# Performance work log

Measured on AMD Instinct MI355X. Metric: run time of the kernel, lower is better.

Reference implementation:

```python
import jax, jax.numpy as jnp
import numpy as np

N_NODES, N_EDGES, BATCH_SIZE = 8192, 65536, 64
N_S, NG, MAX_R = 16, 32, 10.0
SQRT3 = float(np.sqrt(3.0))


def _mlp2(h, w1, b1, w2, b2):
    return jax.nn.relu(h @ w1 + b1) @ w2 + b2


def _mlp3(h, w1, b1, w2, b2, w3, b3):
    h = jax.nn.relu(h @ w1 + b1)
    h = jax.nn.relu(h @ w2 + b2)
    return h @ w3 + b3


def _scatter_mean(vals, idx, n):
    s = jax.ops.segment_sum(vals, idx, num_segments=n)
    c = jax.ops.segment_sum(jnp.ones(vals.shape[:1], vals.dtype), idx, num_segments=n)
    return s / jnp.maximum(c, 1.0)[:, None]


def _forward_molecule(x, pos, src, dst, batch, params):
    (ne_w1, ne_b1, ne_w2, ne_b2, ee_w1, ee_b1, ee_w2, ee_b2,
     c0_w1, c0_b1, c0_w2, c0_b2, c1_w1, c1_b1, c1_w2, c1_b2,
     sn_w1, sn_b1, sn_w2, sn_b2, sn_w3, sn_b3,
     se_w1, se_b1, se_w2, se_b2, se_w3, se_b3) = params
    n = x.shape[0]
    evec = pos[dst] - pos[src]                       # [E,3]
    dist = jnp.sqrt(jnp.sum(evec * evec, -1) + 1e-12)
    mu = jnp.linspace(0.0, MAX_R, NG)
    coeff = -0.5 / (MAX_R / (NG - 1)) ** 2           # GaussianSmearing
    edge_attr = jnp.exp(coeff * (dist[:, None] - mu) ** 2)     # [E,NG]
    sh1 = SQRT3 * evec / dist[:, None]               # l=1 SH, component norm; l=0 part == 1

    h = _mlp2(x, ne_w1, ne_b1, ne_w2, ne_b2)         # node embedding [N,16]
    eemb = _mlp2(edge_attr, ee_w1, ee_b1, ee_w2, ee_b2)        # edge embedding [E,16]

    # ---- conv 0: 16x0e (x) 0e+1o -> 16x0e+16x1o, per-edge TP weights ----
    ea = jnp.concatenate([eemb, h[dst, :N_S], h[src, :N_S]], -1)   # [E,48]
    w = _mlp2(ea, c0_w1, c0_b1, c0_w2, c0_b2)                      # [E,512]
    E = w.shape[0]
    w00 = w[:, :256].reshape(E, 16, 16)    # 0e x 0e -> 0e
    w01 = w[:, 256:].reshape(E, 16, 16)    # 0e x 1o -> 1o
    xs = h[src]
    o0 = 0.25 * jnp.einsum('eu,euw->ew', xs, w00)        # path weight 1/sqrt(16)
    o1 = 0.25 * jnp.einsum('eu,em,euw->ewm', xs, sh1, w01)
    tp = jnp.concatenate([o0, o1.reshape(E, 48)], -1)
    up = _scatter_mean(tp, dst, n)                       # [N,64]
    h = jnp.pad(h, ((0, 0), (0, up.shape[1] - h.shape[1]))) + up

    # ---- conv 1: 16x0e+16x1o (x) 0e+1o -> 16x0e+16x1o+16x1e ----
    ea = jnp.concatenate([eemb, h[dst, :N_S], h[src, :N_S]], -1)
    w = _mlp2(ea, c1_w1, c1_b1, c1_w2, c1_b2)                      # [E,1280]
    wA, wB, wC, wD, wE = (w[:, i * 256:(i + 1) * 256].reshape(E, 16, 16) for i in range(5))
    x0s = h[src, :16]
    x1s = h[src, 16:64].reshape(E, 16, 3)
    pw = 1.0 / float(np.sqrt(32.0))        # two fan-16 paths into 0e and into 1o
    o0 = pw * (jnp.einsum('eu,euw->ew', x0s, wA)
               + jnp.einsum('eui,ei,euw->ew', x1s, sh1, wD) / SQRT3)  # CG(1,1,0)=delta/sqrt3
    o1o = pw * (jnp.einsum('eu,em,euw->ewm', x0s, sh1, wB)
                + jnp.einsum('eum,euw->ewm', x1s, wC))
    cr = jnp.cross(x1s, sh1[:, None, :])                              # CG(1,1,1)=eps/sqrt2
    o1e = (0.25 / float(np.sqrt(2.0))) * jnp.einsum('euk,euw->ewk', cr, wE)
    tp = jnp.concatenate([o0, o1o.reshape(E, 48), o1e.reshape(E, 48)], -1)
    up = _scatter_mean(tp, dst, n)                       # [N,112]
    h = jnp.pad(h, ((0, 0), (0, up.shape[1] - h.shape[1]))) + up

    xf = h[:, :N_S]                                      # n_conv_layers < 3 branch
    s_nodes = _mlp3(xf, sn_w1, sn_b1, sn_w2, sn_b2, sn_w3, sn_b3)   # [N,1]
    s_edges = _mlp3(jnp.concatenate([edge_attr, xf[src], xf[dst]], -1),
                    se_w1, se_b1, se_w2, se_b2, se_w3, se_b3)       # [E,1]
    # edge_in_score=True -> edge and node scatter_add into per-molecule score
    return (jax.ops.segment_sum(s_edges, batch[src], num_segments=BATCH_SIZE)
            + jax.ops.segment_sum(s_nodes, batch, num_segments=BATCH_SIZE))


def setup_inputs() -> dict:
    ks = iter(jax.random.split(jax.random.key(0), 64))

    def nrm(shape, scale=1.0):
        return scale * jax.random.normal(next(ks), shape, jnp.float32)

    def lin(fi, fo):
        return nrm((fi, fo), 1.0 / float(np.sqrt(fi)))

    def z(n):
        return jnp.zeros((n,), jnp.float32)

    inp = {}
    for tag in ('r', 'p'):
        inp[f'x_{tag}'] = nrm((N_NODES, 32))
        inp[f'pos_{tag}'] = 2.0 * jax.random.normal(next(ks), (N_NODES, 3), jnp.float32)
        s = jax.random.randint(next(ks), (N_EDGES,), 0, N_NODES)
        o = jax.random.randint(next(ks), (N_EDGES,), 1, N_NODES)   # no self loops
        inp[f'edge_index_{tag}'] = jnp.stack([s, (s + o) % N_NODES]).astype(jnp.int32)
        inp[f'batch_{tag}'] = jnp.sort(jax.random.randint(next(ks), (N_NODES,), 0, BATCH_SIZE)).astype(jnp.int32)
    inp['ne_w1'] = lin(32, 16); inp['ne_b1'] = z(16); inp['ne_w2'] = lin(16, 16); inp['ne_b2'] = z(16)
    inp['ee_w1'] = lin(32, 16); inp['ee_b1'] = z(16); inp['ee_w2'] = lin(16, 16); inp['ee_b2'] = z(16)
    inp['c0_w1'] = lin(48, 48); inp['c0_b1'] = z(48); inp['c0_w2'] = lin(48, 512); inp['c0_b2'] = z(512)
    inp['c1_w1'] = lin(48, 48); inp['c1_b1'] = z(48); inp['c1_w2'] = lin(48, 1280); inp['c1_b2'] = z(1280)
    inp['sn_w1'] = lin(16, 32); inp['sn_b1'] = z(32); inp['sn_w2'] = lin(32, 16); inp['sn_b2'] = z(16)
    inp['sn_w3'] = lin(16, 1); inp['sn_b3'] = z(1)
    inp['se_w1'] = lin(64, 16); inp['se_b1'] = z(16); inp['se_w2'] = lin(16, 16); inp['se_b2'] = z(16)
    inp['se_w3'] = lin(16, 1); inp['se_b3'] = z(1)
    return inp


def reference(x_r, pos_r, edge_index_r, batch_r, x_p, pos_p, edge_index_p, batch_p,
              ne_w1, ne_b1, ne_w2, ne_b2, ee_w1, ee_b1, ee_w2, ee_b2,
              c0_w1, c0_b1, c0_w2, c0_b2, c1_w1, c1_b1, c1_w2, c1_b2,
              sn_w1, sn_b1, sn_w2, sn_b2, sn_w3, sn_b3,
              se_w1, se_b1, se_w2, se_b2, se_w3, se_b3):
    params = (ne_w1, ne_b1, ne_w2, ne_b2, ee_w1, ee_b1, ee_w2, ee_b2,
              c0_w1, c0_b1, c0_w2, c0_b2, c1_w1, c1_b1, c1_w2, c1_b2,
              sn_w1, sn_b1, sn_w2, sn_b2, sn_w3, sn_b3,
              se_w1, se_b1, se_w2, se_b2, se_w3, se_b3)
    e_r = _forward_molecule(x_r, pos_r, edge_index_r[0], edge_index_r[1], batch_r, params)
    e_p = _forward_molecule(x_p, pos_p, edge_index_p[0], edge_index_p[1], batch_p, params)
    return e_p - e_r   # reaction energy [BATCH_SIZE, 1]
```

## Files before the change

### kernel.cpp

```cpp
#include <hip/hip_runtime.h>
#include <math.h>

#define NN 8192
#define NE 65536
#define SQRT3F 1.7320508075688772f
#define INV_SQRT3F 0.5773502691896258f
#define PW 0.17677669529663687f
#define GSTEP (10.0f/31.0f)
#define GCOEFF (-0.5f/(GSTEP*GSTEP))

typedef _Float16 f16;
typedef f16 f16x2 __attribute__((ext_vector_type(2)));
typedef f16 f16x4 __attribute__((ext_vector_type(4)));
typedef f16 f16x8 __attribute__((ext_vector_type(8)));
typedef float f32x4 __attribute__((ext_vector_type(4)));

#define MFMA(acc, a, b) acc = __builtin_amdgcn_mfma_f32_16x16x32_f16(a, b, acc, 0, 0, 0)

__global__ __launch_bounds__(256) void k_pre(const float* __restrict__ c0w1, const float* __restrict__ c0b1,
                                             const float* __restrict__ c1w1, const float* __restrict__ c1b1,
                                             const float* __restrict__ c0w2, const float* __restrict__ c0b2,
                                             const float* __restrict__ c1w2, const float* __restrict__ c1b2,
                                             f16* __restrict__ w1c0, f16* __restrict__ w1c1,
                                             f16* __restrict__ w2t0, f16* __restrict__ w2t1,
                                             const float* __restrict__ xr, const float* __restrict__ xp,
                                             float* __restrict__ h16f, f16* __restrict__ h16_16,
                                             const float* __restrict__ nw1, const float* __restrict__ nb1,
                                             const float* __restrict__ nw2, const float* __restrict__ nb2,
                                             const int* __restrict__ eir, const int* __restrict__ eip,
                                             const float* __restrict__ posr, const float* __restrict__ posp,
                                             float* __restrict__ sh1d, f16* __restrict__ eemb16,
                                             int* __restrict__ cnt,
                                             const float* __restrict__ ew1, const float* __restrict__ eb1,
                                             const float* __restrict__ ew2, const float* __restrict__ eb2) {
    int b = blockIdx.x;
    int tid = threadIdx.x;
    if (b < 320) {
        int idx = b * 256 + tid;
        if (idx >= 1280 * 64) return;
        int n = idx >> 6, h = idx & 63;
        w2t1[idx] = (f16)((h < 48) ? c1w2[h * 1280 + n] : (h == 48 ? c1b2[n] : 0.f));
        if (n < 512) w2t0[idx] = (f16)((h < 48) ? c0w2[h * 512 + n] : (h == 48 ? c0b2[n] : 0.f));
        if (n < 48) {
            w1c0[idx] = (f16)((h < 48) ? c0w1[h * 48 + n] : (h == 48 ? c0b1[n] : 0.f));
            w1c1[idx] = (f16)((h < 48) ? c1w1[h * 48 + n] : (h == 48 ? c1b1[n] : 0.f));
        }
    } else if (b < 384) {
        int bb = b - 320;
        int mol = bb >> 5;
        const float* x = mol ? xp : xr;
        float* hf = h16f + (size_t)mol * NN * 16;
        f16* h16o = h16_16 + (size_t)mol * NN * 16;
        int v = (bb & 31) * 256 + tid;
        float xi[32];
#pragma unroll
        for (int i = 0; i < 32; i++) xi[i] = x[v * 32 + i];
        float a[16];
#pragma unroll
        for (int j = 0; j < 16; j++) a[j] = nb1[j];
#pragma unroll
        for (int i = 0; i < 32; i++)
#pragma unroll
            for (int j = 0; j < 16; j++) a[j] = fmaf(xi[i], nw1[i * 16 + j], a[j]);
#pragma unroll
        for (int j = 0; j < 16; j++) a[j] = fmaxf(a[j], 0.f);
        float o[16];
#pragma unroll
        for (int j = 0; j < 16; j++) o[j] = nb2[j];
#pragma unroll
        for (int i = 0; i < 16; i++)
#pragma unroll
            for (int j = 0; j < 16; j++) o[j] = fmaf(a[i], nw2[i * 16 + j], o[j]);
#pragma unroll
        for (int j = 0; j < 16; j++) { hf[v * 16 + j] = o[j]; h16o[v * 16 + j] = (f16)o[j]; }
    } else {
        int bb = b - 384;
        int mol = bb >> 8;
        const int* ei = mol ? eip : eir;
        const float* pos = mol ? posp : posr;
        float* sh_ = sh1d + (size_t)mol * NE * 4;
        f16* em_ = eemb16 + (size_t)mol * NE * 16;
        int* cn_ = cnt + mol * NN;
        int e = (bb & 255) * 256 + tid;
        int s = ei[e], d = ei[NE + e];
        float ex = pos[d * 3 + 0] - pos[s * 3 + 0];
        float ey = pos[d * 3 + 1] - pos[s * 3 + 1];
        float ez = pos[d * 3 + 2] - pos[s * 3 + 2];
        float dist = sqrtf(ex * ex + ey * ey + ez * ez + 1e-12f);
        float inv = SQRT3F / dist;
        sh_[e * 4 + 0] = ex * inv;
        sh_[e * 4 + 1] = ey * inv;
        sh_[e * 4 + 2] = ez * inv;
        sh_[e * 4 + 3] = dist;
        float g[32];
#pragma unroll
        for (int i = 0; i < 32; i++) {
            float t = dist - (float)i * GSTEP;
            g[i] = __expf(GCOEFF * t * t);
        }
        float a[16];
#pragma unroll
        for (int j = 0; j < 16; j++) a[j] = eb1[j];
#pragma unroll
        for (int i = 0; i < 32; i++)
#pragma unroll
            for (int j = 0; j < 16; j++) a[j] = fmaf(g[i], ew1[i * 16 + j], a[j]);
#pragma unroll
        for (int j = 0; j < 16; j++) a[j] = fmaxf(a[j], 0.f);
        float o[16];
#pragma unroll
        for (int j = 0; j < 16; j++) o[j] = eb2[j];
#pragma unroll
        for (int i = 0; i < 16; i++)
#pragma unroll
            for (int j = 0; j < 16; j++) o[j] = fmaf(a[i], ew2[i * 16 + j], o[j]);
#pragma unroll
        for (int j = 0; j < 16; j++) em_[e * 16 + j] = (f16)o[j];
        atomicAdd(&cn_[d], 1);
    }
}

__global__ __launch_bounds__(256) void k_scan(int* __restrict__ cnt, int* __restrict__ rowptr,
                                              float* __restrict__ out) {
    __shared__ int part[256];
    int mol = blockIdx.x;
    int* c = cnt + mol * NN;
    int* rp = rowptr + mol * (NN + 1);
    int t = threadIdx.x;
    int base = t * (NN / 256);
    int s = 0;
#pragma unroll
    for (int i = 0; i < NN / 256; i++) s += c[base + i];
    part[t] = s;
    __syncthreads();
    if (t == 0) {
        int run = 0;
        for (int i = 0; i < 256; i++) { int v = part[i]; part[i] = run; run += v; }
    }
    __syncthreads();
    int run = part[t];
    for (int i = 0; i < NN / 256; i++) {
        int cv = c[base + i];
        rp[base + i] = run;
        run += cv;
        c[base + i] = 0;
    }
    if (t == 255) rp[NN] = run;
    if (mol == 0 && t < 64) out[t] = 0.f;
}

__global__ __launch_bounds__(256) void k_fill(const int* __restrict__ eir, const int* __restrict__ eip,
                                              const int* __restrict__ rowptr, int* __restrict__ cnt,
                                              int* __restrict__ eord) {
    int mol = blockIdx.y;
    const int* ei = mol ? eip : eir;
    int e = blockIdx.x * 256 + threadIdx.x;
    int d = ei[NE + e];
    int pos = atomicAdd(&cnt[mol * NN + d], 1);
    eord[mol * NE + rowptr[mol * (NN + 1) + d] + pos] = e;
}

__global__ __launch_bounds__(128) void k_conv0(const int* __restrict__ eir, const int* __restrict__ eip,
                                               const int* __restrict__ eord,
                                               const f16* __restrict__ eemb16, const f16* __restrict__ h16_16,
                                               const float* __restrict__ sh1d,
                                               const f16* __restrict__ w1h, const f16* __restrict__ w2h,
                                               f16* __restrict__ tp0) {
    __shared__ __align__(16) f16 ea[256 * 72];
    __shared__ __align__(16) f16 sc0[256 * 24];
    __shared__ __align__(16) float4 shs[256];
    int mol = blockIdx.y;
    const int* ei = mol ? eip : eir;
    const int* eo = eord + mol * NE;
    const f16* em_ = eemb16 + (size_t)mol * NE * 16;
    const f16* h16_ = h16_16 + (size_t)mol * NN * 16;
    const float* sh_ = sh1d + (size_t)mol * NE * 4;
    f16* tp_ = tp0 + (size_t)mol * NE * 64;
    int tid = threadIdx.x;
    int e0 = blockIdx.x * 256;
#pragma unroll
    for (int ii = 0; ii < 2; ii++) {
        int er = tid * 2 + ii;
        int le = eo[e0 + er];
        int s = ei[le], d = ei[NE + le];
        char* row = (char*)ea + er * 144;
        const f16x8* pe = (const f16x8*)(em_ + (size_t)le * 16);
        ((f16x8*)row)[0] = pe[0]; ((f16x8*)row)[1] = pe[1];
        const f16x8* pd = (const f16x8*)(h16_ + (size_t)d * 16);
        ((f16x8*)row)[2] = pd[0]; ((f16x8*)row)[3] = pd[1];
        const f16x8* ps = (const f16x8*)(h16_ + (size_t)s * 16);
        f16x8 sv0 = ps[0], sv1 = ps[1];
        ((f16x8*)row)[4] = sv0; ((f16x8*)row)[5] = sv1;
        f16x8 z = {}; f16x8 o = {}; o[0] = (f16)1.0f;
        ((f16x8*)row)[6] = o; ((f16x8*)row)[7] = z; ((f16x8*)row)[8] = z;
        char* srow = (char*)sc0 + er * 48;
        *(f16x8*)srow = sv0;
        *(f16x8*)(srow + 16) = sv1;
        shs[er] = *(const float4*)(sh_ + (size_t)le * 4);
    }
    int wv = tid >> 6, l = tid & 63;
    int koff = (l >> 4) * 16;
    int voffB = (l & 15) * 128 + koff;
    int rbase = wv * 128;
#pragma unroll
    for (int t = 0; t < 8; t++) {
        int arow = rbase + t * 16 + (l & 15);
        f16x8 a0 = *(const f16x8*)((const char*)ea + arow * 144 + koff);
        f16x8 a1 = *(const f16x8*)((const char*)ea + arow * 144 + koff + 64);
#pragma unroll
        for (int nt = 0; nt < 3; nt++) {
            f32x4 hacc = {0.f, 0.f, 0.f, 0.f};
            const char* hb = (const char*)w1h + nt * 2048 + voffB;
            MFMA(hacc, a0, *(const f16x8*)(hb));
            MFMA(hacc, a1, *(const f16x8*)(hb + 64));
#pragma unroll
            for (int r = 0; r < 4; r++) {
                int rr = rbase + t * 16 + (l >> 4) * 4 + r;
                ea[rr * 72 + nt * 16 + (l & 15)] = (f16)fmaxf(hacc[r], 0.f);
            }
        }
    }
    f16x8 ha0[8], ha1[8];
#pragma unroll
    for (int t = 0; t < 8; t++) {
        int arow = rbase + t * 16 + (l & 15);
        ha0[t] = *(const f16x8*)((const char*)ea + arow * 144 + koff);
        ha1[t] = *(const f16x8*)((const char*)ea + arow * 144 + koff + 64);
    }
    f32x4 accA[8] = {}, accB[8] = {};
    const char* wB = (const char*)w2h + voffB;
    f16x8 cA0 = *(const f16x8*)(wB), cA1 = *(const f16x8*)(wB + 64);
    f16x8 cB0 = *(const f16x8*)(wB + 32768), cB1 = *(const f16x8*)(wB + 32768 + 64);
#pragma unroll 4
    for (int u = 0; u < 16; ++u) {
        int un = (u < 15) ? u + 1 : 15;
        const char* Hb = wB + un * 2048;
        f16x8 nA0 = *(const f16x8*)(Hb), nA1 = *(const f16x8*)(Hb + 64);
        f16x8 nB0 = *(const f16x8*)(Hb + 32768), nB1 = *(const f16x8*)(Hb + 32768 + 64);
#pragma unroll
        for (int t = 0; t < 8; t++) {
            f16 s = *(const f16*)((const char*)sc0 + (rbase + t * 16 + (l & 15)) * 48 + u * 2);
            f16x8 x0 = ha0[t] * s, x1 = ha1[t] * s;
            MFMA(accA[t], x0, cA0); MFMA(accA[t], x1, cA1);
            MFMA(accB[t], x0, cB0); MFMA(accB[t], x1, cB1);
        }
        cA0 = nA0; cA1 = nA1; cB0 = nB0; cB1 = nB1;
    }
    int w = l & 15;
#pragma unroll
    for (int t = 0; t < 8; t++)
#pragma unroll
        for (int r = 0; r < 4; r++) {
            int ro = rbase + t * 16 + (l >> 4) * 4 + r;
            int i = e0 + ro;
            float4 shv = shs[ro];
            f16* tpp = tp_ + (size_t)i * 64;
            float tb = 0.25f * accB[t][r];
            tpp[w] = (f16)(0.25f * accA[t][r]);
            tpp[16 + w] = (f16)(tb * shv.x);
            tpp[32 + w] = (f16)(tb * shv.y);
            tpp[48 + w] = (f16)(tb * shv.z);
        }
}

__global__ __launch_bounds__(256) void k_up0g(const float* __restrict__ h16f, const f16* __restrict__ tp0,
                                              const int* __restrict__ rowptr,
                                              float* __restrict__ h64f, f16* __restrict__ h64_16) {
    int mol = blockIdx.y;
    const float* h_ = h16f + (size_t)mol * NN * 16;
    const f16* tp = tp0 + (size_t)mol * NE * 64;
    const int* rp = rowptr + mol * (NN + 1);
    float* o_ = h64f + (size_t)mol * NN * 64;
    f16* o16_ = h64_16 + (size_t)mol * NN * 16;
    int tid = threadIdx.x;
    int v = blockIdx.x * 64 + (tid >> 2), q = tid & 3;
    int r0 = rp[v], r1 = rp[v + 1];
    float acc[16];
#pragma unroll
    for (int j = 0; j < 16; j++) acc[j] = 0.f;
    for (int i = r0; i < r1; i++) {
        const f16* src = tp + (size_t)i * 64 + q * 16;
        f16x8 v0 = *(const f16x8*)src;
        f16x8 v1 = *(const f16x8*)(src + 8);
#pragma unroll
        for (int j = 0; j < 8; j++) { acc[j] += (float)v0[j]; acc[8 + j] += (float)v1[j]; }
    }
    float rc = 1.0f / fmaxf((float)(r1 - r0), 1.0f);
    if (q == 0) {
#pragma unroll
        for (int w = 0; w < 16; w++) {
            float val = fmaf(acc[w], rc, h_[(size_t)v * 16 + w]);
            o_[(size_t)v * 64 + w] = val;
            o16_[(size_t)v * 16 + w] = (f16)val;
        }
    } else {
#pragma unroll
        for (int w = 0; w < 16; w++) o_[(size_t)v * 64 + 16 + 3 * w + (q - 1)] = acc[w] * rc;
    }
}

__global__ __launch_bounds__(128) void k_conv1(const int* __restrict__ eir, const int* __restrict__ eip,
                                               const int* __restrict__ eord,
                                               const f16* __restrict__ eemb16, const f16* __restrict__ h64_16,
                                               const float* __restrict__ h64f, const float* __restrict__ sh1d,
                                               const f16* __restrict__ w1h, const f16* __restrict__ w2h,
                                               f16* __restrict__ tp1) {
    __shared__ __align__(16) f16 ea[256 * 72];
    __shared__ __align__(16) f16 sc1[256 * 36];
    int mol = blockIdx.y;
    const int* ei = mol ? eip : eir;
    const int* eo = eord + mol * NE;
    const f16* em_ = eemb16 + (size_t)mol * NE * 16;
    const f16* h16_ = h64_16 + (size_t)mol * NN * 16;
    const float* hf_ = h64f + (size_t)mol * NN * 64;
    const float* sh_ = sh1d + (size_t)mol * NE * 4;
    f16* tp_ = tp1 + (size_t)mol * NE * 16;
    int tid = threadIdx.x;
    int e0 = blockIdx.x * 256;
#pragma unroll
    for (int ii = 0; ii < 2; ii++) {
        int er = tid * 2 + ii;
        int le = eo[e0 + er];
        int s = ei[le], d = ei[NE + le];
        char* row = (char*)ea + er * 144;
        const f16x8* pe = (const f16x8*)(em_ + (size_t)le * 16);
        ((f16x8*)row)[0] = pe[0]; ((f16x8*)row)[1] = pe[1];
        const f16x8* pd = (const f16x8*)(h16_ + (size_t)d * 16);
        ((f16x8*)row)[2] = pd[0]; ((f16x8*)row)[3] = pd[1];
        const f16x8* ps = (const f16x8*)(h16_ + (size_t)s * 16);
        ((f16x8*)row)[4] = ps[0]; ((f16x8*)row)[5] = ps[1];
        f16x8 z = {}; f16x8 o = {}; o[0] = (f16)1.0f;
        ((f16x8*)row)[6] = o; ((f16x8*)row)[7] = z; ((f16x8*)row)[8] = z;
        float4 shv = *(const float4*)(sh_ + (size_t)le * 4);
        const float* hfs = hf_ + (size_t)s * 64;
        float xu[16];
#pragma unroll
        for (int g = 0; g < 4; g++) {
            float4 v4 = *(const float4*)(hfs + g * 4);
            xu[g * 4 + 0] = v4.x; xu[g * 4 + 1] = v4.y; xu[g * 4 + 2] = v4.z; xu[g * 4 + 3] = v4.w;
        }
        float x1v[48];
#pragma unroll
        for (int g = 0; g < 12; g++) {
            float4 v4 = *(const float4*)(hfs + 16 + g * 4);
            x1v[g * 4 + 0] = v4.x; x1v[g * 4 + 1] = v4.y; x1v[g * 4 + 2] = v4.z; x1v[g * 4 + 3] = v4.w;
        }
        char* srow = (char*)sc1 + er * 72;
#pragma unroll
        for (int g = 0; g < 4; g++) {
            f16x8 pk;
#pragma unroll
            for (int k2 = 0; k2 < 4; k2++) {
                int k = g * 4 + k2;
                float du = (x1v[k * 3] * shv.x + x1v[k * 3 + 1] * shv.y + x1v[k * 3 + 2] * shv.z) * INV_SQRT3F;
                pk[k2 * 2 + 0] = (f16)xu[k];
                pk[k2 * 2 + 1] = (f16)du;
            }
            *(f16x8*)(srow + g * 16) = pk;
        }
    }
    int wv = tid >> 6, l = tid & 63;
    int koff = (l >> 4) * 16;
    int voffB = (l & 15) * 128 + koff;
    int rbase = wv * 128;
#pragma unroll
    for (int t = 0; t < 8; t++) {
        int arow = rbase + t * 16 + (l & 15);
        f16x8 a0 = *(const f16x8*)((const char*)ea + arow * 144 + koff);
        f16x8 a1 = *(const f16x8*)((const char*)ea + arow * 144 + koff + 64);
#pragma unroll
        for (int nt = 0; nt < 3; nt++) {
            f32x4 hacc = {0.f, 0.f, 0.f, 0.f};
            const char* hb = (const char*)w1h + nt * 2048 + voffB;
            MFMA(hacc, a0, *(const f16x8*)(hb));
            MFMA(hacc, a1, *(const f16x8*)(hb + 64));
#pragma unroll
            for (int r = 0; r < 4; r++) {
                int rr = rbase + t * 16 + (l >> 4) * 4 + r;
                ea[rr * 72 + nt * 16 + (l & 15)] = (f16)fmaxf(hacc[r], 0.f);
            }
        }
    }
    f16x8 ha0[8], ha1[8];
#pragma unroll
    for (int t = 0; t < 8; t++) {
        int arow = rbase + t * 16 + (l & 15);
        ha0[t] = *(const f16x8*)((const char*)ea + arow * 144 + koff);
        ha1[t] = *(const f16x8*)((const char*)ea + arow * 144 + koff + 64);
    }
    f32x4 accA[8] = {};
    const char* wB = (const char*)w2h + voffB;
    f16x8 cA0 = *(const f16x8*)(wB), cA1 = *(const f16x8*)(wB + 64);
    f16x8 cD0 = *(const f16x8*)(wB + 98304), cD1 = *(const f16x8*)(wB + 98304 + 64);
#pragma unroll 4
    for (int u = 0; u < 16; ++u) {
        int un = (u < 15) ? u + 1 : 15;
        const char* Hb = wB + un * 2048;
        f16x8 nA0 = *(const f16x8*)(Hb), nA1 = *(const f16x8*)(Hb + 64);
        f16x8 nD0 = *(const f16x8*)(Hb + 98304), nD1 = *(const f16x8*)(Hb + 98304 + 64);
#pragma unroll
        for (int t = 0; t < 8; t++) {
            f16x2 sp = *(const f16x2*)((const char*)sc1 + (rbase + t * 16 + (l & 15)) * 72 + u * 4);
            f16x8 x0 = ha0[t] * sp[0], x1 = ha1[t] * sp[0];
            MFMA(accA[t], x0, cA0); MFMA(accA[t], x1, cA1);
            x0 = ha0[t] * sp[1]; x1 = ha1[t] * sp[1];
            MFMA(accA[t], x0, cD0); MFMA(accA[t], x1, cD1);
        }
        cA0 = nA0; cA1 = nA1; cD0 = nD0; cD1 = nD1;
    }
    int w = l & 15;
#pragma unroll
    for (int t = 0; t < 8; t++)
#pragma unroll
        for (int r = 0; r < 4; r++) {
            int i = e0 + rbase + t * 16 + (l >> 4) * 4 + r;
            tp_[(size_t)i * 16 + w] = (f16)(PW * accA[t][r]);
        }
}

__global__ __launch_bounds__(256) void k_xfg(const float* __restrict__ h64f, const f16* __restrict__ tp1,
                                             const int* __restrict__ rowptr,
                                             float* __restrict__ xf,
                                             const int* __restrict__ batchr, const int* __restrict__ batchp,
                                             const float* __restrict__ w1, const float* __restrict__ b1,
                                             const float* __restrict__ w2, const float* __restrict__ b2,
                                             const float* __restrict__ w3, const float* __restrict__ b3,
                                             float* __restrict__ out) {
    __shared__ float xfs[64][17];
    __shared__ float buck[64];
    int tid = threadIdx.x;
    if (tid < 64) buck[tid] = 0.f;
    int mol = blockIdx.y;
    float sign = mol ? 1.f : -1.f;
    const int* batch = mol ? batchp : batchr;
    const float* h_ = h64f + (size_t)mol * NN * 64;
    const f16* tp = tp1 + (size_t)mol * NE * 16;
    const int* rp = rowptr + mol * (NN + 1);
    float* xf_ = xf + (size_t)mol * NN * 16;
    int v = blockIdx.x * 64 + (tid >> 2), q = tid & 3;
    int r0 = rp[v], r1 = rp[v + 1];
    float a0 = 0.f, a1 = 0.f, a2 = 0.f, a3 = 0.f;
    for (int i = r0; i < r1; i++) {
        f16x4 t4 = *(const f16x4*)(tp + (size_t)i * 16 + q * 4);
        a0 += (float)t4[0]; a1 += (float)t4[1]; a2 += (float)t4[2]; a3 += (float)t4[3];
    }
    float rc = 1.0f / fmaxf((float)(r1 - r0), 1.0f);
    float4 hv = *(const float4*)(h_ + (size_t)v * 64 + q * 4);
    float4 xv4;
    xv4.x = fmaf(a0, rc, hv.x); xv4.y = fmaf(a1, rc, hv.y);
    xv4.z = fmaf(a2, rc, hv.z); xv4.w = fmaf(a3, rc, hv.w);
    xfs[tid >> 2][q * 4 + 0] = xv4.x; xfs[tid >> 2][q * 4 + 1] = xv4.y;
    xfs[tid >> 2][q * 4 + 2] = xv4.z; xfs[tid >> 2][q * 4 + 3] = xv4.w;
    *(float4*)(xf_ + (size_t)v * 16 + q * 4) = xv4;
    __syncthreads();
    if (tid < 64) {
        int v2 = blockIdx.x * 64 + tid;
        float xv[16];
#pragma unroll
        for (int c = 0; c < 16; c++) xv[c] = xfs[tid][c];
        float aa[32];
#pragma unroll
        for (int j = 0; j < 32; j++) aa[j] = b1[j];
#pragma unroll
        for (int i = 0; i < 16; i++)
#pragma unroll
            for (int j = 0; j < 32; j++) aa[j] = fmaf(xv[i], w1[i * 32 + j], aa[j]);
#pragma unroll
        for (int j = 0; j < 32; j++) aa[j] = fmaxf(aa[j], 0.f);
        float bb[16];
#pragma unroll
        for (int j = 0; j < 16; j++) bb[j] = b2[j];
#pragma unroll
        for (int i = 0; i < 32; i++)
#pragma unroll
            for (int j = 0; j < 16; j++) bb[j] = fmaf(aa[i], w2[i * 16 + j], bb[j]);
#pragma unroll
        for (int j = 0; j < 16; j++) bb[j] = fmaxf(bb[j], 0.f);
        float val = b3[0];
#pragma unroll
        for (int i = 0; i < 16; i++) val = fmaf(bb[i], w3[i], val);
        atomicAdd(&buck[batch[v2]], val);
    }
    __syncthreads();
    if (tid < 64) atomicAdd(&out[tid], sign * buck[tid]);
}

__global__ __launch_bounds__(256) void k_sedge(const int* __restrict__ eir, const int* __restrict__ eip,
                                               const int* __restrict__ batchr, const int* __restrict__ batchp,
                                               const float* __restrict__ sh1d, const float* __restrict__ xf,
                                               const float* __restrict__ w1, const float* __restrict__ b1,
                                               const float* __restrict__ w2, const float* __restrict__ b2,
                                               const float* __restrict__ w3, const float* __restrict__ b3,
                                               float* __restrict__ out) {
    __shared__ float buck[64];
    int tid = threadIdx.x;
    if (tid < 64) buck[tid] = 0.f;
    __syncthreads();
    int mol = blockIdx.y;
    float sign = mol ? 1.f : -1.f;
    const int* ei = mol ? eip : eir;
    const int* batch = mol ? batchp : batchr;
    const float* sh_ = sh1d + (size_t)mol * NE * 4;
    const float* xf_ = xf + (size_t)mol * NN * 16;
    int e = blockIdx.x * 256 + tid;
    int s = ei[e], d = ei[NE + e];
    float dist = sh_[e * 4 + 3];
    float in[64];
#pragma unroll
    for (int i = 0; i < 32; i++) {
        float t = dist - (float)i * GSTEP;
        in[i] = __expf(GCOEFF * t * t);
    }
#pragma unroll
    for (int i = 0; i < 16; i++) in[32 + i] = xf_[s * 16 + i];
#pragma unroll
    for (int i = 0; i < 16; i++) in[48 + i] = xf_[d * 16 + i];
    float a[16];
#pragma unroll
    for (int j = 0; j < 16; j++) a[j] = b1[j];
#pragma unroll
    for (int i = 0; i < 64; i++)
#pragma unroll
        for (int j = 0; j < 16; j++) a[j] = fmaf(in[i], w1[i * 16 + j], a[j]);
#pragma unroll
    for (int j = 0; j < 16; j++) a[j] = fmaxf(a[j], 0.f);
    float bb[16];
#pragma unroll
    for (int j = 0; j < 16; j++) bb[j] = b2[j];
#pragma unroll
    for (int i = 0; i < 16; i++)
#pragma unroll
        for (int j = 0; j < 16; j++) bb[j] = fmaf(a[i], w2[i * 16 + j], bb[j]);
#pragma unroll
    for (int j = 0; j < 16; j++) bb[j] = fmaxf(bb[j], 0.f);
    float val = b3[0];
#pragma unroll
    for (int i = 0; i < 16; i++) val = fmaf(bb[i], w3[i], val);
    atomicAdd(&buck[batch[s]], val);
    __syncthreads();
    if (tid < 64) atomicAdd(&out[tid], sign * buck[tid]);
}

extern "C" void kernel_launch(void* const* d_in, const int* in_sizes, int n_in,
                              void* d_out, int out_size, void* d_ws, size_t ws_size,
                              hipStream_t stream) {
    const float* x_r = (const float*)d_in[0];
    const float* pos_r = (const float*)d_in[1];
    const int* ei_r = (const int*)d_in[2];
    const int* batch_r = (const int*)d_in[3];
    const float* x_p = (const float*)d_in[4];
    const float* pos_p = (const float*)d_in[5];
    const int* ei_p = (const int*)d_in[6];
    const int* batch_p = (const int*)d_in[7];
    const float* ne_w1 = (const float*)d_in[8];
    const float* ne_b1 = (const float*)d_in[9];
    const float* ne_w2 = (const float*)d_in[10];
    const float* ne_b2 = (const float*)d_in[11];
    const float* ee_w1 = (const float*)d_in[12];
    const float* ee_b1 = (const float*)d_in[13];
    const float* ee_w2 = (const float*)d_in[14];
    const float* ee_b2 = (const float*)d_in[15];
    const float* c0_w1 = (const float*)d_in[16];
    const float* c0_b1 = (const float*)d_in[17];
    const float* c0_w2 = (const float*)d_in[18];
    const float* c0_b2 = (const float*)d_in[19];
    const float* c1_w1 = (const float*)d_in[20];
    const float* c1_b1 = (const float*)d_in[21];
    const float* c1_w2 = (const float*)d_in[22];
    const float* c1_b2 = (const float*)d_in[23];
    const float* sn_w1 = (const float*)d_in[24];
    const float* sn_b1 = (const float*)d_in[25];
    const float* sn_w2 = (const float*)d_in[26];
    const float* sn_b2 = (const float*)d_in[27];
    const float* sn_w3 = (const float*)d_in[28];
    const float* sn_b3 = (const float*)d_in[29];
    const float* se_w1 = (const float*)d_in[30];
    const float* se_b1 = (const float*)d_in[31];
    const float* se_w2 = (const float*)d_in[32];
    const float* se_b2 = (const float*)d_in[33];
    const float* se_w3 = (const float*)d_in[34];
    const float* se_b3 = (const float*)d_in[35];
    float* out = (float*)d_out;

    char* p = (char*)d_ws;
    auto alloc = [&](size_t bytes) { char* r = p; p += (bytes + 255) & ~(size_t)255; return r; };
    f16* w2t1 = (f16*)alloc(1280 * 64 * 2);
    f16* w2t0 = (f16*)alloc(512 * 64 * 2);
    f16* w1c0 = (f16*)alloc(48 * 64 * 2);
    f16* w1c1 = (f16*)alloc(48 * 64 * 2);
    f16* eemb16 = (f16*)alloc((size_t)2 * NE * 16 * 2);
    f16* h16_16 = (f16*)alloc((size_t)2 * NN * 16 * 2);
    f16* h64_16 = (f16*)alloc((size_t)2 * NN * 16 * 2);
    float* h16f = (float*)alloc((size_t)2 * NN * 16 * 4);
    float* sh1d = (float*)alloc((size_t)2 * NE * 4 * 4);
    int* cntI = (int*)alloc((size_t)2 * NN * 4);
    int* rowptr = (int*)alloc((size_t)2 * (NN + 1) * 4);
    int* eord = (int*)alloc((size_t)2 * NE * 4);
    f16* tp0 = (f16*)alloc((size_t)2 * NE * 64 * 2);
    f16* tp1 = tp0;
    float* h64f = (float*)alloc((size_t)2 * NN * 64 * 4);
    float* xf = (float*)alloc((size_t)2 * NN * 16 * 4);
    (void)ws_size; (void)n_in; (void)in_sizes; (void)out_size;

    hipMemsetAsync(cntI, 0, (size_t)2 * NN * 4, stream);

    dim3 blk256(256, 1, 1), blk128(128, 1, 1);
    dim3 ge(NE / 256, 2, 1);
    dim3 gc(NE / 256, 2, 1);

    k_pre<<<dim3(896, 1, 1), blk256, 0, stream>>>(c0_w1, c0_b1, c1_w1, c1_b1, c0_w2, c0_b2, c1_w2, c1_b2,
                                                  w1c0, w1c1, w2t0, w2t1,
                                                  x_r, x_p, h16f, h16_16, ne_w1, ne_b1, ne_w2, ne_b2,
                                                  ei_r, ei_p, pos_r, pos_p, sh1d, eemb16, cntI,
                                                  ee_w1, ee_b1, ee_w2, ee_b2);
    k_scan<<<dim3(2, 1, 1), blk256, 0, stream>>>(cntI, rowptr, out);
    k_fill<<<ge, blk256, 0, stream>>>(ei_r, ei_p, rowptr, cntI, eord);
    k_conv0<<<gc, blk128, 0, stream>>>(ei_r, ei_p, eord, eemb16, h16_16, sh1d, w1c0, w2t0, tp0);
    k_up0g<<<dim3(NN / 64, 2, 1), blk256, 0, stream>>>(h16f, tp0, rowptr, h64f, h64_16);
    k_conv1<<<gc, blk128, 0, stream>>>(ei_r, ei_p, eord, eemb16, h64_16, h64f, sh1d, w1c1, w2t1, tp1);
    k_xfg<<<dim3(NN / 64, 2, 1), blk256, 0, stream>>>(h64f, tp1, rowptr, xf, batch_r, batch_p,
                                                      sn_w1, sn_b1, sn_w2, sn_b2, sn_w3, sn_b3, out);
    k_sedge<<<ge, blk256, 0, stream>>>(ei_r, ei_p, batch_r, batch_p, sh1d, xf,
                                       se_w1, se_b1, se_w2, se_b2, se_w3, se_b3, out);
}
```

Measured before the change: 147.8 us.

## Fuse scan into fill kernel and store node features in fp16

Merges the CSR scan and fill kernels into one launch: every block redundantly recomputes the prefix sum into shared memory, which removes one launch and the rowptr round trip. Block 0 still writes the global rowptr, and a separate zeroed counter array replaces reusing cnt. Node features h64 and the final xf are stored as fp16 instead of fp32, which halves gather traffic in conv1 and the edge readout. The risks are the redundant scan work in each of 512 blocks, a 32KB shared buffer that limits occupancy, and lower precision in the gathered features.

```diff
diff --git a/kernel.cpp b/kernel.cpp
--- a/kernel.cpp
+++ b/kernel.cpp
@@ -120,44 +120,50 @@
     }
 }
 
-__global__ __launch_bounds__(256) void k_scan(int* __restrict__ cnt, int* __restrict__ rowptr,
-                                              float* __restrict__ out) {
+__global__ __launch_bounds__(256) void k_fillscan(const int* __restrict__ eir, const int* __restrict__ eip,
+                                                  const int* __restrict__ cnt, int* __restrict__ fillc,
+                                                  int* __restrict__ rowptr, int* __restrict__ eord,
+                                                  float* __restrict__ out) {
+    __shared__ int rpl[NN];
     __shared__ int part[256];
-    int mol = blockIdx.x;
-    int* c = cnt + mol * NN;
-    int* rp = rowptr + mol * (NN + 1);
-    int t = threadIdx.x;
-    int base = t * (NN / 256);
+    int mol = blockIdx.y;
+    int cb = blockIdx.x;
+    int tid = threadIdx.x;
+    const int* c = cnt + mol * NN;
+    int base = tid * (NN / 256);
     int s = 0;
 #pragma unroll
     for (int i = 0; i < NN / 256; i++) s += c[base + i];
-    part[t] = s;
+    part[tid] = s;
     __syncthreads();
-    if (t == 0) {
+    if (tid == 0) {
         int run = 0;
         for (int i = 0; i < 256; i++) { int v = part[i]; part[i] = run; run += v; }
     }
     __syncthreads();
-    int run = part[t];
-    for (int i = 0; i < NN / 256; i++) {
-        int cv = c[base + i];
-        rp[base + i] = run;
-        run += cv;
-        c[base + i] = 0;
-    }
-    if (t == 255) rp[NN] = run;
-    if (mol == 0 && t < 64) out[t] = 0.f;
-}
-
-__global__ __launch_bounds__(256) void k_fill(const int* __restrict__ eir, const int* __restrict__ eip,
-                                              const int* __restrict__ rowptr, int* __restrict__ cnt,
-                                              int* __restrict__ eord) {
-    int mol = blockIdx.y;
+    {
+        int run = part[tid];
+        for (int i = 0; i < NN / 256; i++) {
+            rpl[base + i] = run;
+            run += c[base + i];
+        }
+        if (cb == 0) {
+            int r2 = part[tid];
+            int* rp = rowptr + mol * (NN + 1);
+            for (int i = 0; i < NN / 256; i++) {
+                rp[base + i] = r2;
+                r2 += c[base + i];
+            }
+            if (tid == 255) rp[NN] = r2;
+            if (mol == 0 && tid < 64) out[tid] = 0.f;
+        }
+    }
+    __syncthreads();
     const int* ei = mol ? eip : eir;
-    int e = blockIdx.x * 256 + threadIdx.x;
+    int e = cb * 256 + tid;
     int d = ei[NE + e];
-    int pos = atomicAdd(&cnt[mol * NN + d], 1);
-    eord[mol * NE + rowptr[mol * (NN + 1) + d] + pos] = e;
+    int pos = atomicAdd(&fillc[mol * NN + d], 1);
+    eord[mol * NE + rpl[d] + pos] = e;
 }
 
 __global__ __launch_bounds__(128) void k_conv0(const int* __restrict__ eir, const int* __restrict__ eip,
@@ -265,13 +271,13 @@
 
 __global__ __launch_bounds__(256) void k_up0g(const float* __restrict__ h16f, const f16* __restrict__ tp0,
                                               const int* __restrict__ rowptr,
-                                              float* __restrict__ h64f, f16* __restrict__ h64_16) {
+                                              f16* __restrict__ h64_16, float* __restrict__ h0f) {
     int mol = blockIdx.y;
     const float* h_ = h16f + (size_t)mol * NN * 16;
     const f16* tp = tp0 + (size_t)mol * NE * 64;
     const int* rp = rowptr + mol * (NN + 1);
-    float* o_ = h64f + (size_t)mol * NN * 64;
-    f16* o16_ = h64_16 + (size_t)mol * NN * 16;
+    f16* o16_ = h64_16 + (size_t)mol * NN * 64;
+    float* o0_ = h0f + (size_t)mol * NN * 16;
     int tid = threadIdx.x;
     int v = blockIdx.x * 64 + (tid >> 2), q = tid & 3;
     int r0 = rp[v], r1 = rp[v + 1];
@@ -290,19 +296,19 @@
 #pragma unroll
         for (int w = 0; w < 16; w++) {
             float val = fmaf(acc[w], rc, h_[(size_t)v * 16 + w]);
-            o_[(size_t)v * 64 + w] = val;
-            o16_[(size_t)v * 16 + w] = (f16)val;
+            o0_[(size_t)v * 16 + w] = val;
+            o16_[(size_t)v * 64 + w] = (f16)val;
         }
     } else {
 #pragma unroll
-        for (int w = 0; w < 16; w++) o_[(size_t)v * 64 + 16 + 3 * w + (q - 1)] = acc[w] * rc;
+        for (int w = 0; w < 16; w++) o16_[(size_t)v * 64 + 16 + 3 * w + (q - 1)] = (f16)(acc[w] * rc);
     }
 }
 
 __global__ __launch_bounds__(128) void k_conv1(const int* __restrict__ eir, const int* __restrict__ eip,
                                                const int* __restrict__ eord,
                                                const f16* __restrict__ eemb16, const f16* __restrict__ h64_16,
-                                               const float* __restrict__ h64f, const float* __restrict__ sh1d,
+                                               const float* __restrict__ sh1d,
                                                const f16* __restrict__ w1h, const f16* __restrict__ w2h,
                                                f16* __restrict__ tp1) {
     __shared__ __align__(16) f16 ea[256 * 72];
@@ -311,8 +317,7 @@
     const int* ei = mol ? eip : eir;
     const int* eo = eord + mol * NE;
     const f16* em_ = eemb16 + (size_t)mol * NE * 16;
-    const f16* h16_ = h64_16 + (size_t)mol * NN * 16;
-    const float* hf_ = h64f + (size_t)mol * NN * 64;
+    const f16* h64_ = h64_16 + (size_t)mol * NN * 64;
     const float* sh_ = sh1d + (size_t)mol * NE * 4;
     f16* tp_ = tp1 + (size_t)mol * NE * 16;
     int tid = threadIdx.x;
@@ -325,25 +330,24 @@
         char* row = (char*)ea + er * 144;
         const f16x8* pe = (const f16x8*)(em_ + (size_t)le * 16);
         ((f16x8*)row)[0] = pe[0]; ((f16x8*)row)[1] = pe[1];
-        const f16x8* pd = (const f16x8*)(h16_ + (size_t)d * 16);
+        const f16x8* pd = (const f16x8*)(h64_ + (size_t)d * 64);
         ((f16x8*)row)[2] = pd[0]; ((f16x8*)row)[3] = pd[1];
-        const f16x8* ps = (const f16x8*)(h16_ + (size_t)s * 16);
-        ((f16x8*)row)[4] = ps[0]; ((f16x8*)row)[5] = ps[1];
+        const f16* hs = h64_ + (size_t)s * 64;
+        const f16x8* ps = (const f16x8*)hs;
+        f16x8 hs0 = ps[0], hs1 = ps[1];
+        ((f16x8*)row)[4] = hs0; ((f16x8*)row)[5] = hs1;
         f16x8 z = {}; f16x8 o = {}; o[0] = (f16)1.0f;
         ((f16x8*)row)[6] = o; ((f16x8*)row)[7] = z; ((f16x8*)row)[8] = z;
         float4 shv = *(const float4*)(sh_ + (size_t)le * 4);
-        const float* hfs = hf_ + (size_t)s * 64;
         float xu[16];
 #pragma unroll
-        for (int g = 0; g < 4; g++) {
-            float4 v4 = *(const float4*)(hfs + g * 4);
-            xu[g * 4 + 0] = v4.x; xu[g * 4 + 1] = v4.y; xu[g * 4 + 2] = v4.z; xu[g * 4 + 3] = v4.w;
-        }
+        for (int j = 0; j < 8; j++) { xu[j] = (float)hs0[j]; xu[8 + j] = (float)hs1[j]; }
         float x1v[48];
 #pragma unroll
-        for (int g = 0; g < 12; g++) {
-            float4 v4 = *(const float4*)(hfs + 16 + g * 4);
-            x1v[g * 4 + 0] = v4.x; x1v[g * 4 + 1] = v4.y; x1v[g * 4 + 2] = v4.z; x1v[g * 4 + 3] = v4.w;
+        for (int g = 0; g < 6; g++) {
+            f16x8 v8 = ps[2 + g];
+#pragma unroll
+            for (int j = 0; j < 8; j++) x1v[g * 8 + j] = (float)v8[j];
         }
         char* srow = (char*)sc1 + er * 72;
 #pragma unroll
@@ -418,9 +422,9 @@
         }
 }
 
-__global__ __launch_bounds__(256) void k_xfg(const float* __restrict__ h64f, const f16* __restrict__ tp1,
+__global__ __launch_bounds__(256) void k_xfg(const float* __restrict__ h0f, const f16* __restrict__ tp1,
                                              const int* __restrict__ rowptr,
-                                             float* __restrict__ xf,
+                                             f16* __restrict__ xf16,
                                              const int* __restrict__ batchr, const int* __restrict__ batchp,
                                              const float* __restrict__ w1, const float* __restrict__ b1,
                                              const float* __restrict__ w2, const float* __restrict__ b2,
@@ -433,10 +437,10 @@
     int mol = blockIdx.y;
     float sign = mol ? 1.f : -1.f;
     const int* batch = mol ? batchp : batchr;
-    const float* h_ = h64f + (size_t)mol * NN * 64;
+    const float* h_ = h0f + (size_t)mol * NN * 16;
     const f16* tp = tp1 + (size_t)mol * NE * 16;
     const int* rp = rowptr + mol * (NN + 1);
-    float* xf_ = xf + (size_t)mol * NN * 16;
+    f16* xf_ = xf16 + (size_t)mol * NN * 16;
     int v = blockIdx.x * 64 + (tid >> 2), q = tid & 3;
     int r0 = rp[v], r1 = rp[v + 1];
     float a0 = 0.f, a1 = 0.f, a2 = 0.f, a3 = 0.f;
@@ -445,13 +449,13 @@
         a0 += (float)t4[0]; a1 += (float)t4[1]; a2 += (float)t4[2]; a3 += (float)t4[3];
     }
     float rc = 1.0f / fmaxf((float)(r1 - r0), 1.0f);
-    float4 hv = *(const float4*)(h_ + (size_t)v * 64 + q * 4);
-    float4 xv4;
-    xv4.x = fmaf(a0, rc, hv.x); xv4.y = fmaf(a1, rc, hv.y);
-    xv4.z = fmaf(a2, rc, hv.z); xv4.w = fmaf(a3, rc, hv.w);
-    xfs[tid >> 2][q * 4 + 0] = xv4.x; xfs[tid >> 2][q * 4 + 1] = xv4.y;
-    xfs[tid >> 2][q * 4 + 2] = xv4.z; xfs[tid >> 2][q * 4 + 3] = xv4.w;
-    *(float4*)(xf_ + (size_t)v * 16 + q * 4) = xv4;
+    float4 hv = *(const float4*)(h_ + (size_t)v * 16 + q * 4);
+    float x0 = fmaf(a0, rc, hv.x), x1 = fmaf(a1, rc, hv.y);
+    float x2 = fmaf(a2, rc, hv.z), x3 = fmaf(a3, rc, hv.w);
+    xfs[tid >> 2][q * 4 + 0] = x0; xfs[tid >> 2][q * 4 + 1] = x1;
+    xfs[tid >> 2][q * 4 + 2] = x2; xfs[tid >> 2][q * 4 + 3] = x3;
+    f16x4 xo = {(f16)x0, (f16)x1, (f16)x2, (f16)x3};
+    *(f16x4*)(xf_ + (size_t)v * 16 + q * 4) = xo;
     __syncthreads();
     if (tid < 64) {
         int v2 = blockIdx.x * 64 + tid;
@@ -487,7 +491,7 @@
 
 __global__ __launch_bounds__(256) void k_sedge(const int* __restrict__ eir, const int* __restrict__ eip,
                                                const int* __restrict__ batchr, const int* __restrict__ batchp,
-                                               const float* __restrict__ sh1d, const float* __restrict__ xf,
+                                               const float* __restrict__ sh1d, const f16* __restrict__ xf16,
                                                const float* __restrict__ w1, const float* __restrict__ b1,
                                                const float* __restrict__ w2, const float* __restrict__ b2,
                                                const float* __restrict__ w3, const float* __restrict__ b3,
@@ -501,7 +505,7 @@
     const int* ei = mol ? eip : eir;
     const int* batch = mol ? batchp : batchr;
     const float* sh_ = sh1d + (size_t)mol * NE * 4;
-    const float* xf_ = xf + (size_t)mol * NN * 16;
+    const f16* xf_ = xf16 + (size_t)mol * NN * 16;
     int e = blockIdx.x * 256 + tid;
     int s = ei[e], d = ei[NE + e];
     float dist = sh_[e * 4 + 3];
@@ -511,10 +515,17 @@
         float t = dist - (float)i * GSTEP;
         in[i] = __expf(GCOEFF * t * t);
     }
-#pragma unroll
-    for (int i = 0; i < 16; i++) in[32 + i] = xf_[s * 16 + i];
-#pragma unroll
-    for (int i = 0; i < 16; i++) in[48 + i] = xf_[d * 16 + i];
+    {
+        f16x8 s0v = *(const f16x8*)(xf_ + (size_t)s * 16);
+        f16x8 s1v = *(const f16x8*)(xf_ + (size_t)s * 16 + 8);
+        f16x8 d0v = *(const f16x8*)(xf_ + (size_t)d * 16);
+        f16x8 d1v = *(const f16x8*)(xf_ + (size_t)d * 16 + 8);
+#pragma unroll
+        for (int i = 0; i < 8; i++) {
+            in[32 + i] = (float)s0v[i]; in[40 + i] = (float)s1v[i];
+            in[48 + i] = (float)d0v[i]; in[56 + i] = (float)d1v[i];
+        }
+    }
     float a[16];
 #pragma unroll
     for (int j = 0; j < 16; j++) a[j] = b1[j];
@@ -590,19 +601,20 @@
     f16* w1c1 = (f16*)alloc(48 * 64 * 2);
     f16* eemb16 = (f16*)alloc((size_t)2 * NE * 16 * 2);
     f16* h16_16 = (f16*)alloc((size_t)2 * NN * 16 * 2);
-    f16* h64_16 = (f16*)alloc((size_t)2 * NN * 16 * 2);
+    f16* h64_16 = (f16*)alloc((size_t)2 * NN * 64 * 2);
     float* h16f = (float*)alloc((size_t)2 * NN * 16 * 4);
     float* sh1d = (float*)alloc((size_t)2 * NE * 4 * 4);
     int* cntI = (int*)alloc((size_t)2 * NN * 4);
+    int* fillc = (int*)alloc((size_t)2 * NN * 4);
     int* rowptr = (int*)alloc((size_t)2 * (NN + 1) * 4);
     int* eord = (int*)alloc((size_t)2 * NE * 4);
     f16* tp0 = (f16*)alloc((size_t)2 * NE * 64 * 2);
     f16* tp1 = tp0;
-    float* h64f = (float*)alloc((size_t)2 * NN * 64 * 4);
-    float* xf = (float*)alloc((size_t)2 * NN * 16 * 4);
+    float* h0f = (float*)alloc((size_t)2 * NN * 16 * 4);
+    f16* xf16 = (f16*)alloc((size_t)2 * NN * 16 * 2);
     (void)ws_size; (void)n_in; (void)in_sizes; (void)out_size;
 
-    hipMemsetAsync(cntI, 0, (size_t)2 * NN * 4, stream);
+    hipMemsetAsync(cntI, 0, (size_t)2 * NN * 4 * 2, stream);
 
     dim3 blk256(256, 1, 1), blk128(128, 1, 1);
     dim3 ge(NE / 256, 2, 1);
@@ -613,13 +625,12 @@
                                                   x_r, x_p, h16f, h16_16, ne_w1, ne_b1, ne_w2, ne_b2,
                                                   ei_r, ei_p, pos_r, pos_p, sh1d, eemb16, cntI,
                                                   ee_w1, ee_b1, ee_w2, ee_b2);
-    k_scan<<<dim3(2, 1, 1), blk256, 0, stream>>>(cntI, rowptr, out);
-    k_fill<<<ge, blk256, 0, stream>>>(ei_r, ei_p, rowptr, cntI, eord);
+    k_fillscan<<<ge, blk256, 0, stream>>>(ei_r, ei_p, cntI, fillc, rowptr, eord, out);
     k_conv0<<<gc, blk128, 0, stream>>>(ei_r, ei_p, eord, eemb16, h16_16, sh1d, w1c0, w2t0, tp0);
-    k_up0g<<<dim3(NN / 64, 2, 1), blk256, 0, stream>>>(h16f, tp0, rowptr, h64f, h64_16);
-    k_conv1<<<gc, blk128, 0, stream>>>(ei_r, ei_p, eord, eemb16, h64_16, h64f, sh1d, w1c1, w2t1, tp1);
-    k_xfg<<<dim3(NN / 64, 2, 1), blk256, 0, stream>>>(h64f, tp1, rowptr, xf, batch_r, batch_p,
+    k_up0g<<<dim3(NN / 64, 2, 1), blk256, 0, stream>>>(h16f, tp0, rowptr, h64_16, h0f);
+    k_conv1<<<gc, blk128, 0, stream>>>(ei_r, ei_p, eord, eemb16, h64_16, sh1d, w1c1, w2t1, tp1);
+    k_xfg<<<dim3(NN / 64, 2, 1), blk256, 0, stream>>>(h0f, tp1, rowptr, xf16, batch_r, batch_p,
                                                       sn_w1, sn_b1, sn_w2, sn_b2, sn_w3, sn_b3, out);
-    k_sedge<<<ge, blk256, 0, stream>>>(ei_r, ei_p, batch_r, batch_p, sh1d, xf,
+    k_sedge<<<ge, blk256, 0, stream>>>(ei_r, ei_p, batch_r, batch_p, sh1d, xf16,
                                        se_w1, se_b1, se_w2, se_b2, se_w3, se_b3, out);
 }
```

Measured after the change: 143.0 us, median of 2. 1.03x faster.
